# Kernel tuning notes

Hardware: AMD Instinct MI355X
Metric: run time of the kernel (lower is better)

Reference implementation:

```python
import jax, jax.numpy as jnp
import numpy as np

VOCAB = 100000
D = 128
B = 256
L = 2048  # leaves per tree (power of two -> complete binary tree)


def setup_inputs() -> dict:
    key = jax.random.key(0)
    k1, k2, k3, k4 = jax.random.split(key, 4)
    word_ids = jax.random.randint(k1, (B, L), 0, VOCAB)
    embedding = jax.random.normal(k2, (VOCAB, D), dtype=jnp.float32) * 0.1
    # torch nn.Linear(2*D, D): weight [D, 2*D], bias [D]
    W = jax.random.normal(k3, (D, 2 * D), dtype=jnp.float32) * (1.0 / np.sqrt(2 * D))
    b = jax.random.normal(k4, (D,), dtype=jnp.float32) * 0.01
    return {"word_ids": word_ids, "embedding": embedding, "W": W, "b": b}


def reference(word_ids, embedding, W, b):
    # Leaves: embedding lookup for every leaf of every tree. [B, L, D]
    x = embedding[word_ids]
    # Internal nodes, batched by depth: each level combines adjacent pairs
    # via linear(concat(left, right)). log2(L) levels (static unroll).
    while x.shape[1] > 1:
        left = x[:, 0::2, :]   # [B, n/2, D]
        right = x[:, 1::2, :]  # [B, n/2, D]
        pair = jnp.concatenate([left, right], axis=-1)  # [B, n/2, 2D]
        x = jnp.einsum('bnd,od->bno', pair, W) + b      # [B, n/2, D]
    return x[:, 0, :]  # root result per tree, [B, D]
```

## Files before the change

kernel.cpp:

```cpp
#include <hip/hip_runtime.h>


typedef __bf16 bf16x8 __attribute__((ext_vector_type(8)));
typedef __bf16 bf16x4 __attribute__((ext_vector_type(4)));
typedef float f32x4 __attribute__((ext_vector_type(4)));

#define NROWS 144

__device__ __forceinline__ int sw_off(int row, int col) {
    return row * 128 + ((((col >> 3) ^ (row & 15)) << 3) | (col & 7));
}

__global__ void pack_w_kernel(const float* __restrict__ W,
                              __bf16* __restrict__ wpack) {
    const int gf = blockIdx.x;
    const int l = threadIdx.x;
    const int nt = gf >> 3, kk = gf & 7;
    const int o = nt * 16 + (l & 15);
    const int d = kk * 32 + ((l >> 4) << 3);
    const float* src = W + o * 256 + d;
    bf16x8 h;
#pragma unroll
    for (int j = 0; j < 8; ++j) h[j] = (__bf16)src[j];
    *(bf16x8*)(wpack + (size_t)(gf * 64 + l) * 8) = h;
}

template <int NOUT, int MODE>
__device__ __forceinline__ void step(
    __bf16* __restrict__ L, int off, int dstb,
    const bf16x8* wf, const float* bval, int wv, int q, int lm)
{
    const int me = (NOUT >= 16) ? lm : (lm < NOUT ? lm : 0);
    f32x4 acc[2];
    acc[0] = (f32x4){ bval[0], bval[0], bval[0], bval[0] };
    acc[1] = (f32x4){ bval[1], bval[1], bval[1], bval[1] };
#pragma unroll
    for (int kk = 0; kk < 8; ++kk) {
        const int j = 2 * me + (kk >> 2);
        const int row = MODE ? (j < 16 ? 128 + j : j - 16) : off + j;
        const int col = (kk & 3) * 32 + q * 8;
        const bf16x8 af = *(const bf16x8*)&L[sw_off(row, col)];
        acc[0] = __builtin_amdgcn_mfma_f32_16x16x32_bf16(af, wf[kk],     acc[0], 0, 0, 0);
        acc[1] = __builtin_amdgcn_mfma_f32_16x16x32_bf16(af, wf[8 + kk], acc[1], 0, 0, 0);
    }
#pragma unroll
    for (int nl = 0; nl < 2; ++nl) {
        const int col = (2 * wv + nl) * 16 + lm;
        const bf16x4 hv = __builtin_convertvector(acc[nl], bf16x4);
#pragma unroll
        for (int r = 0; r < 4; ++r) {
            const int row = q * 4 + r;
            if (NOUT >= 16 || row < NOUT)
                L[sw_off(dstb + row, col)] = hv[r];
        }
    }
}

__device__ __forceinline__ void step8_to_global(
    const __bf16* __restrict__ L, int off, __bf16* __restrict__ yrow,
    const bf16x8* wf, const float* bval, int wv, int q, int lm)
{
    const int me = (lm < 8) ? lm : 0;
    f32x4 acc[2];
    acc[0] = (f32x4){ bval[0], bval[0], bval[0], bval[0] };
    acc[1] = (f32x4){ bval[1], bval[1], bval[1], bval[1] };
#pragma unroll
    for (int kk = 0; kk < 8; ++kk) {
        const int j = 2 * me + (kk >> 2);
        const int col = (kk & 3) * 32 + q * 8;
        const bf16x8 af = *(const bf16x8*)&L[sw_off(off + j, col)];
        acc[0] = __builtin_amdgcn_mfma_f32_16x16x32_bf16(af, wf[kk],     acc[0], 0, 0, 0);
        acc[1] = __builtin_amdgcn_mfma_f32_16x16x32_bf16(af, wf[8 + kk], acc[1], 0, 0, 0);
    }
#pragma unroll
    for (int nl = 0; nl < 2; ++nl) {
        const int col = (2 * wv + nl) * 16 + lm;
#pragma unroll
        for (int r = 0; r < 4; ++r) {
            const int row = q * 4 + r;
            if (row < 8)
                yrow[(size_t)row * 128 + col] = (__bf16)acc[nl][r];
        }
    }
}

__global__ __launch_bounds__(256) void tree128_kernel(
    const int* __restrict__ wid, const float* __restrict__ emb,
    const __bf16* __restrict__ wpack, const float* __restrict__ bias,
    __bf16* __restrict__ yout)
{
    __shared__ __align__(16) __bf16 L[NROWS * 128];
    const int tid = threadIdx.x;
    const int batch = blockIdx.x >> 4;
    const int grp = blockIdx.x & 15;
    const int wv = tid >> 6, ln = tid & 63, q = ln >> 4, lm = ln & 15;

    {
        const int* wb = wid + batch * 2048 + grp * 128;
        int idreg[16];
#pragma unroll
        for (int i = 0; i < 16; ++i) idreg[i] = wb[(tid >> 5) + 8 * i];
#pragma unroll
        for (int i = 0; i < 16; ++i) {
            const int row = (tid >> 5) + 8 * i;
            const int c4 = tid & 31;
            const f32x4 v =
                *(const f32x4*)(emb + (size_t)idreg[i] * 128 + c4 * 4);
            *(bf16x4*)&L[sw_off(row, c4 * 4)] =
                __builtin_convertvector(v, bf16x4);
        }
    }

    bf16x8 wf[16];
    const bf16x8* wp = (const bf16x8*)wpack;
#pragma unroll
    for (int f = 0; f < 16; ++f) wf[f] = wp[(16 * wv + f) * 64 + ln];
    float bval[2];
    bval[0] = bias[(2 * wv + 0) * 16 + lm];
    bval[1] = bias[(2 * wv + 1) * 16 + lm];

    __syncthreads();
    step<16, 0>(L, 0, 128, wf, bval, wv, q, lm);
    __syncthreads();
    step<16, 0>(L, 32, 0, wf, bval, wv, q, lm);
    __syncthreads();
    step<16, 0>(L, 64, 16, wf, bval, wv, q, lm);
    step<16, 0>(L, 96, 32, wf, bval, wv, q, lm);
    __syncthreads();
    step<16, 1>(L, 0, 48, wf, bval, wv, q, lm);
    step<16, 0>(L, 16, 64, wf, bval, wv, q, lm);
    __syncthreads();
    step<16, 0>(L, 48, 0, wf, bval, wv, q, lm);
    __syncthreads();
    step8_to_global(L, 0, yout + (size_t)(batch * 128 + grp * 8) * 128,
                    wf, bval, wv, q, lm);
}

__global__ __launch_bounds__(256) void finish_kernel(
    const __bf16* __restrict__ yin, const __bf16* __restrict__ wpack,
    const float* __restrict__ bias, float* __restrict__ out)
{
    __shared__ __align__(16) __bf16 L[NROWS * 128];
    const int tid = threadIdx.x;
    const int batch = blockIdx.x;
    const int wv = tid >> 6, ln = tid & 63, q = ln >> 4, lm = ln & 15;

    bf16x8 wf[16];
    const bf16x8* wp = (const bf16x8*)wpack;
#pragma unroll
    for (int f = 0; f < 16; ++f) wf[f] = wp[(16 * wv + f) * 64 + ln];
    float bval[2];
    bval[0] = bias[(2 * wv + 0) * 16 + lm];
    bval[1] = bias[(2 * wv + 1) * 16 + lm];

#pragma unroll
    for (int i = 0; i < 8; ++i) {
        const int flat = tid + 256 * i;
        const int row = flat >> 4;
        const int c8 = flat & 15;
        const bf16x8 v =
            *(const bf16x8*)(yin + (size_t)(batch * 128 + row) * 128 + c8 * 8);
        *(bf16x8*)&L[sw_off(row, c8 * 8)] = v;
    }
    __syncthreads();

    step<16, 0>(L, 0, 128, wf, bval, wv, q, lm);
    __syncthreads();
    step<16, 0>(L, 32, 0, wf, bval, wv, q, lm);
    __syncthreads();
    step<16, 0>(L, 64, 16, wf, bval, wv, q, lm);
    step<16, 0>(L, 96, 32, wf, bval, wv, q, lm);
    __syncthreads();
    step<16, 1>(L, 0, 48, wf, bval, wv, q, lm);
    step<16, 0>(L, 16, 64, wf, bval, wv, q, lm);
    __syncthreads();
    step<16, 0>(L, 48, 0, wf, bval, wv, q, lm);
    __syncthreads();
    step<8, 0>(L, 0, 16, wf, bval, wv, q, lm);
    __syncthreads();
    step<4, 0>(L, 16, 0, wf, bval, wv, q, lm);
    __syncthreads();
    step<2, 0>(L, 0, 8, wf, bval, wv, q, lm);
    __syncthreads();

    {
        f32x4 acc[2];
        acc[0] = (f32x4){ bval[0], bval[0], bval[0], bval[0] };
        acc[1] = (f32x4){ bval[1], bval[1], bval[1], bval[1] };
#pragma unroll
        for (int kk = 0; kk < 8; ++kk) {
            const int row = 8 + (kk >> 2);
            const int col = (kk & 3) * 32 + q * 8;
            const bf16x8 af = *(const bf16x8*)&L[sw_off(row, col)];
            acc[0] = __builtin_amdgcn_mfma_f32_16x16x32_bf16(af, wf[kk],     acc[0], 0, 0, 0);
            acc[1] = __builtin_amdgcn_mfma_f32_16x16x32_bf16(af, wf[8 + kk], acc[1], 0, 0, 0);
        }
        if (q == 0) {
#pragma unroll
            for (int nl = 0; nl < 2; ++nl)
                out[(size_t)batch * 128 + (2 * wv + nl) * 16 + lm] = acc[nl][0];
        }
    }
}

extern "C" void kernel_launch(void* const* d_in, const int* in_sizes, int n_in,
                              void* d_out, int out_size, void* d_ws, size_t ws_size,
                              hipStream_t stream) {
    const int*   wid = (const int*)d_in[0];
    const float* emb = (const float*)d_in[1];
    const float* W   = (const float*)d_in[2];
    const float* b   = (const float*)d_in[3];
    float* out = (float*)d_out;

    __bf16* wpack = (__bf16*)d_ws;
    __bf16* y     = wpack + 32768;

    pack_w_kernel<<<64, 64, 0, stream>>>(W, wpack);
    tree128_kernel<<<4096, 256, 0, stream>>>(wid, emb, wpack, b, y);
    finish_kernel<<<256, 256, 0, stream>>>(y, wpack, b, out);
}
```

Measured before the change: 149.1 us.

## Reduce deeper in first kernel, padded LDS stride, double-buffered finish tree

The 128-leaf kernel now runs two extra levels and emits 2 nodes per block instead of 8, so the intermediate buffer and the finish kernel's load shrink fourfold. The finish kernel becomes a 32-input loop that ping-pongs between two LDS buffers. Shared-memory addressing switches from an XOR swizzle to a padded row stride of 136 elements to avoid bank conflicts. This shifts more tiny, poorly utilized MFMA levels into the wide first kernel and may change LDS conflict behavior.

```diff
diff --git a/kernel.cpp b/kernel.cpp
--- a/kernel.cpp
+++ b/kernel.cpp
@@ -5,11 +5,8 @@
 typedef __bf16 bf16x4 __attribute__((ext_vector_type(4)));
 typedef float f32x4 __attribute__((ext_vector_type(4)));
 
+#define STRIDE 136
 #define NROWS 144
-
-__device__ __forceinline__ int sw_off(int row, int col) {
-    return row * 128 + ((((col >> 3) ^ (row & 15)) << 3) | (col & 7));
-}
 
 __global__ void pack_w_kernel(const float* __restrict__ W,
                               __bf16* __restrict__ wpack) {
@@ -39,7 +36,7 @@
         const int j = 2 * me + (kk >> 2);
         const int row = MODE ? (j < 16 ? 128 + j : j - 16) : off + j;
         const int col = (kk & 3) * 32 + q * 8;
-        const bf16x8 af = *(const bf16x8*)&L[sw_off(row, col)];
+        const bf16x8 af = *(const bf16x8*)&L[row * STRIDE + col];
         acc[0] = __builtin_amdgcn_mfma_f32_16x16x32_bf16(af, wf[kk],     acc[0], 0, 0, 0);
         acc[1] = __builtin_amdgcn_mfma_f32_16x16x32_bf16(af, wf[8 + kk], acc[1], 0, 0, 0);
     }
@@ -51,35 +48,33 @@
         for (int r = 0; r < 4; ++r) {
             const int row = q * 4 + r;
             if (NOUT >= 16 || row < NOUT)
-                L[sw_off(dstb + row, col)] = hv[r];
-        }
-    }
-}
-
-__device__ __forceinline__ void step8_to_global(
+                L[(dstb + row) * STRIDE + col] = hv[r];
+        }
+    }
+}
+
+__device__ __forceinline__ void final_tile(
     const __bf16* __restrict__ L, int off, __bf16* __restrict__ yrow,
     const bf16x8* wf, const float* bval, int wv, int q, int lm)
 {
-    const int me = (lm < 8) ? lm : 0;
+    const int me = (lm < 2) ? lm : 0;
     f32x4 acc[2];
     acc[0] = (f32x4){ bval[0], bval[0], bval[0], bval[0] };
     acc[1] = (f32x4){ bval[1], bval[1], bval[1], bval[1] };
 #pragma unroll
     for (int kk = 0; kk < 8; ++kk) {
-        const int j = 2 * me + (kk >> 2);
+        const int row = off + 2 * me + (kk >> 2);
         const int col = (kk & 3) * 32 + q * 8;
-        const bf16x8 af = *(const bf16x8*)&L[sw_off(off + j, col)];
+        const bf16x8 af = *(const bf16x8*)&L[row * STRIDE + col];
         acc[0] = __builtin_amdgcn_mfma_f32_16x16x32_bf16(af, wf[kk],     acc[0], 0, 0, 0);
         acc[1] = __builtin_amdgcn_mfma_f32_16x16x32_bf16(af, wf[8 + kk], acc[1], 0, 0, 0);
     }
 #pragma unroll
     for (int nl = 0; nl < 2; ++nl) {
         const int col = (2 * wv + nl) * 16 + lm;
-#pragma unroll
-        for (int r = 0; r < 4; ++r) {
-            const int row = q * 4 + r;
-            if (row < 8)
-                yrow[(size_t)row * 128 + col] = (__bf16)acc[nl][r];
+        if (q == 0) {
+            yrow[0 * 128 + col] = (__bf16)acc[nl][0];
+            yrow[1 * 128 + col] = (__bf16)acc[nl][1];
         }
     }
 }
@@ -89,7 +84,7 @@
     const __bf16* __restrict__ wpack, const float* __restrict__ bias,
     __bf16* __restrict__ yout)
 {
-    __shared__ __align__(16) __bf16 L[NROWS * 128];
+    __shared__ __align__(16) __bf16 L[NROWS * STRIDE];
     const int tid = threadIdx.x;
     const int batch = blockIdx.x >> 4;
     const int grp = blockIdx.x & 15;
@@ -106,7 +101,7 @@
             const int c4 = tid & 31;
             const f32x4 v =
                 *(const f32x4*)(emb + (size_t)idreg[i] * 128 + c4 * 4);
-            *(bf16x4*)&L[sw_off(row, c4 * 4)] =
+            *(bf16x4*)&L[row * STRIDE + c4 * 4] =
                 __builtin_convertvector(v, bf16x4);
         }
     }
@@ -132,15 +127,19 @@
     __syncthreads();
     step<16, 0>(L, 48, 0, wf, bval, wv, q, lm);
     __syncthreads();
-    step8_to_global(L, 0, yout + (size_t)(batch * 128 + grp * 8) * 128,
-                    wf, bval, wv, q, lm);
-}
-
-__global__ __launch_bounds__(256) void finish_kernel(
+    step<8, 0>(L, 0, 16, wf, bval, wv, q, lm);
+    __syncthreads();
+    step<4, 0>(L, 16, 0, wf, bval, wv, q, lm);
+    __syncthreads();
+    final_tile(L, 0, yout + (size_t)(batch * 32 + grp * 2) * 128,
+               wf, bval, wv, q, lm);
+}
+
+__global__ __launch_bounds__(256) void tree32_kernel(
     const __bf16* __restrict__ yin, const __bf16* __restrict__ wpack,
     const float* __restrict__ bias, float* __restrict__ out)
 {
-    __shared__ __align__(16) __bf16 L[NROWS * 128];
+    __shared__ __align__(16) __bf16 buf[2][32 * STRIDE];
     const int tid = threadIdx.x;
     const int batch = blockIdx.x;
     const int wv = tid >> 6, ln = tid & 63, q = ln >> 4, lm = ln & 15;
@@ -154,52 +153,50 @@
     bval[1] = bias[(2 * wv + 1) * 16 + lm];
 
 #pragma unroll
-    for (int i = 0; i < 8; ++i) {
+    for (int i = 0; i < 2; ++i) {
         const int flat = tid + 256 * i;
         const int row = flat >> 4;
         const int c8 = flat & 15;
         const bf16x8 v =
-            *(const bf16x8*)(yin + (size_t)(batch * 128 + row) * 128 + c8 * 8);
-        *(bf16x8*)&L[sw_off(row, c8 * 8)] = v;
-    }
-    __syncthreads();
-
-    step<16, 0>(L, 0, 128, wf, bval, wv, q, lm);
-    __syncthreads();
-    step<16, 0>(L, 32, 0, wf, bval, wv, q, lm);
-    __syncthreads();
-    step<16, 0>(L, 64, 16, wf, bval, wv, q, lm);
-    step<16, 0>(L, 96, 32, wf, bval, wv, q, lm);
-    __syncthreads();
-    step<16, 1>(L, 0, 48, wf, bval, wv, q, lm);
-    step<16, 0>(L, 16, 64, wf, bval, wv, q, lm);
-    __syncthreads();
-    step<16, 0>(L, 48, 0, wf, bval, wv, q, lm);
-    __syncthreads();
-    step<8, 0>(L, 0, 16, wf, bval, wv, q, lm);
-    __syncthreads();
-    step<4, 0>(L, 16, 0, wf, bval, wv, q, lm);
-    __syncthreads();
-    step<2, 0>(L, 0, 8, wf, bval, wv, q, lm);
-    __syncthreads();
-
-    {
-        f32x4 acc[2];
-        acc[0] = (f32x4){ bval[0], bval[0], bval[0], bval[0] };
-        acc[1] = (f32x4){ bval[1], bval[1], bval[1], bval[1] };
+            *(const bf16x8*)(yin + (size_t)(batch * 32 + row) * 128 + c8 * 8);
+        *(bf16x8*)&buf[0][row * STRIDE + c8 * 8] = v;
+    }
+    __syncthreads();
+
+    int nin = 32, rb = 0;
+    while (nin > 1) {
+        const int nout = nin >> 1;
+        const int me = (lm < nout) ? lm : 0;
+        bf16x8 af[8];
 #pragma unroll
         for (int kk = 0; kk < 8; ++kk) {
-            const int row = 8 + (kk >> 2);
+            const int hi = kk >> 2;
             const int col = (kk & 3) * 32 + q * 8;
-            const bf16x8 af = *(const bf16x8*)&L[sw_off(row, col)];
-            acc[0] = __builtin_amdgcn_mfma_f32_16x16x32_bf16(af, wf[kk],     acc[0], 0, 0, 0);
-            acc[1] = __builtin_amdgcn_mfma_f32_16x16x32_bf16(af, wf[8 + kk], acc[1], 0, 0, 0);
-        }
-        if (q == 0) {
-#pragma unroll
-            for (int nl = 0; nl < 2; ++nl)
-                out[(size_t)batch * 128 + (2 * wv + nl) * 16 + lm] = acc[nl][0];
-        }
+            af[kk] = *(const bf16x8*)&buf[rb][(2 * me + hi) * STRIDE + col];
+        }
+#pragma unroll
+        for (int nl = 0; nl < 2; ++nl) {
+            f32x4 acc = { bval[nl], bval[nl], bval[nl], bval[nl] };
+#pragma unroll
+            for (int kk = 0; kk < 8; ++kk)
+                acc = __builtin_amdgcn_mfma_f32_16x16x32_bf16(
+                    af[kk], wf[nl * 8 + kk], acc, 0, 0, 0);
+            const int col = (2 * wv + nl) * 16 + lm;
+            if (nout == 1) {
+                if (q == 0) out[(size_t)batch * 128 + col] = acc[0];
+            } else {
+                const bf16x4 hv = __builtin_convertvector(acc, bf16x4);
+#pragma unroll
+                for (int r = 0; r < 4; ++r) {
+                    const int row = q * 4 + r;
+                    if (row < nout)
+                        buf[rb ^ 1][row * STRIDE + col] = hv[r];
+                }
+            }
+        }
+        __syncthreads();
+        rb ^= 1;
+        nin = nout;
     }
 }
 
@@ -217,5 +214,5 @@
 
     pack_w_kernel<<<64, 64, 0, stream>>>(W, wpack);
     tree128_kernel<<<4096, 256, 0, stream>>>(wid, emb, wpack, b, y);
-    finish_kernel<<<256, 256, 0, stream>>>(y, wpack, b, out);
-}
+    tree32_kernel<<<256, 256, 0, stream>>>(y, wpack, b, out);
+}
```

Result: faster. 146.0 us (-2.1%).
